# Kernel tuning notes

Hardware: AMD Instinct MI355X
Metric: run time of the kernel (lower is better)

## Reference

```python
import jax, jax.numpy as jnp
import numpy as np

TIME_STEP = 15
INIT_STATE = 0.01  # torch.full((B,H), 0.01)


def setup_inputs() -> dict:
    key = jax.random.key(0)
    k1, k2, k3, k4, k5 = jax.random.split(key, 5)
    B, IN, H = 2048, 2048, 1024
    scale_ih = 1.0 / np.sqrt(H)
    return {
        "x": jax.random.normal(k1, (B, IN), dtype=jnp.float32),
        "W_ih": jax.random.normal(k2, (4 * H, IN), dtype=jnp.float32) * scale_ih,
        "W_hh": jax.random.normal(k3, (4 * H, H), dtype=jnp.float32) * scale_ih,
        "b_ih": jax.random.normal(k4, (4 * H,), dtype=jnp.float32) * scale_ih,
        "b_hh": jax.random.normal(k5, (4 * H,), dtype=jnp.float32) * scale_ih,
    }


def reference(x, W_ih, W_hh, b_ih, b_hh):
    B = x.shape[0]
    H = W_hh.shape[1]
    # x is constant across steps -> precompute input-gate contribution once
    xg = x @ W_ih.T + b_ih  # [B, 4H]
    h0 = jnp.full((B, H), INIT_STATE, dtype=x.dtype)
    c0 = jnp.full((B, H), INIT_STATE, dtype=x.dtype)

    def step(carry, _):
        h, c = carry
        gates = xg + h @ W_hh.T + b_hh  # [B, 4H]
        i, f, g, o = jnp.split(gates, 4, axis=-1)
        i = jax.nn.sigmoid(i)
        f = jax.nn.sigmoid(f)
        g = jnp.tanh(g)
        o = jax.nn.sigmoid(o)
        c_new = f * c + i * g
        h_new = o * jnp.tanh(c_new)
        return (h_new, c_new), h_new

    _, hs = jax.lax.scan(step, (h0, c0), None, length=TIME_STEP)
    return hs  # [T, B, H]
```

## Files before the change

### kernel.cpp

```cpp
#include <hip/hip_runtime.h>
#include <hip/hip_bf16.h>

typedef float f32x4 __attribute__((ext_vector_type(4)));
typedef __bf16 bf16x8 __attribute__((ext_vector_type(8)));

#define B_SZ 2048
#define IN_SZ 2048
#define H_SZ 1024
#define G_SZ (4 * H_SZ)
#define T_STEPS 15
#define INIT_ST 0.01f

__device__ __forceinline__ float sigmoid_f(float x) { return 1.0f / (1.0f + __expf(-x)); }
__device__ __forceinline__ float tanh_f(float x)    { return 1.0f - 2.0f / (__expf(2.0f * x) + 1.0f); }

__device__ __forceinline__ void split8(f32x4 v0, f32x4 v1, bf16x8* h, bf16x8* l) {
  bf16x8 hv, lv;
  #pragma unroll
  for (int j = 0; j < 4; ++j) {
    float f = v0[j];
    __bf16 hb = (__bf16)f;
    hv[j] = hb;
    lv[j] = (__bf16)(f - (float)hb);
  }
  #pragma unroll
  for (int j = 0; j < 4; ++j) {
    float f = v1[j];
    __bf16 hb = (__bf16)f;
    hv[4 + j] = hb;
    lv[4 + j] = (__bf16)(f - (float)hb);
  }
  *h = hv;
  *l = lv;
}

__device__ __forceinline__ bf16x8 cvt8(f32x4 v0, f32x4 v1) {
  bf16x8 hv;
  #pragma unroll
  for (int j = 0; j < 4; ++j) hv[j] = (__bf16)v0[j];
  #pragma unroll
  for (int j = 0; j < 4; ++j) hv[4 + j] = (__bf16)v1[j];
  return hv;
}

__device__ __forceinline__ void gl16(const bf16x8* src, bf16x8* lds_base_uniform) {
  __builtin_amdgcn_global_load_lds(
      (const __attribute__((address_space(1))) void*)src,
      (__attribute__((address_space(3))) void*)lds_base_uniform, 16, 0, 0);
}

__global__ __launch_bounds__(256)
void repack_whh(const float* __restrict__ Whh, bf16x8* __restrict__ Wh)
{
  int cid = blockIdx.x * 256 + threadIdx.x;
  int s    = cid & 1023;
  int rest = cid >> 10;
  int ks   = rest & 31;
  int nt   = rest >> 5;
  int row  = s >> 2;
  int kc   = (s & 3) ^ (row & 3);
  int gate = row >> 6, col = row & 63;
  const float* src = Whh + (size_t)(gate * H_SZ + nt * 64 + col) * H_SZ + ks * 32 + kc * 8;
  Wh[cid] = cvt8(*(const f32x4*)src, *(const f32x4*)(src + 4));
}

__global__ __launch_bounds__(256)
void init_h0(bf16x8* __restrict__ hh, bf16x8* __restrict__ hl)
{
  int cid = blockIdx.x * 256 + threadIdx.x;
  __bf16 hi = (__bf16)INIT_ST;
  __bf16 lo = (__bf16)(INIT_ST - (float)hi);
  bf16x8 h, l;
  #pragma unroll
  for (int j = 0; j < 8; ++j) { h[j] = hi; l[j] = lo; }
  hh[cid] = h;
  hl[cid] = l;
}

__global__ __launch_bounds__(256, 2)
void xg_gemm(const float* __restrict__ x, const float* __restrict__ Wih,
             const float* __restrict__ bih, const float* __restrict__ bhh,
             float* __restrict__ xg)
{
  __shared__ bf16x8 Ah[128 * 4], Al[128 * 4], Bh[128 * 4], Bl[128 * 4];
  const int tid  = threadIdx.x;
  const int lane = tid & 63;
  const int wv   = tid >> 6;
  const int wm   = wv >> 1, wn = wv & 1;
  const int bm   = blockIdx.y * 128;
  const int bn   = blockIdx.x * 128;

  f32x4 acc[4][4] = {};

  for (int k0 = 0; k0 < IN_SZ; k0 += 32) {
    #pragma unroll
    for (int c = 0; c < 2; ++c) {
      int cid = tid + c * 256;
      int row = cid >> 2, kc = cid & 3;
      int idx = row * 4 + (kc ^ (row & 3));
      const float* srcA = x + (size_t)(bm + row) * IN_SZ + k0 + kc * 8;
      split8(*(const f32x4*)srcA, *(const f32x4*)(srcA + 4), &Ah[idx], &Al[idx]);
      const float* srcB = Wih + (size_t)(bn + row) * IN_SZ + k0 + kc * 8;
      split8(*(const f32x4*)srcB, *(const f32x4*)(srcB + 4), &Bh[idx], &Bl[idx]);
    }
    __syncthreads();

    const int kc = lane >> 4;
    bf16x8 ah[4], al[4], bh[4], bl[4];
    #pragma unroll
    for (int i = 0; i < 4; ++i) {
      int ra = wm * 64 + i * 16 + (lane & 15);
      int ia = ra * 4 + (kc ^ (ra & 3));
      ah[i] = Ah[ia]; al[i] = Al[ia];
      int rb = wn * 64 + i * 16 + (lane & 15);
      int ib = rb * 4 + (kc ^ (rb & 3));
      bh[i] = Bh[ib]; bl[i] = Bl[ib];
    }
    #pragma unroll
    for (int i = 0; i < 4; ++i)
      #pragma unroll
      for (int j = 0; j < 4; ++j) {
        acc[i][j] = __builtin_amdgcn_mfma_f32_16x16x32_bf16(ah[i], bh[j], acc[i][j], 0, 0, 0);
        acc[i][j] = __builtin_amdgcn_mfma_f32_16x16x32_bf16(ah[i], bl[j], acc[i][j], 0, 0, 0);
        acc[i][j] = __builtin_amdgcn_mfma_f32_16x16x32_bf16(al[i], bh[j], acc[i][j], 0, 0, 0);
      }
    __syncthreads();
  }

  #pragma unroll
  for (int i = 0; i < 4; ++i) {
    int m0 = bm + wm * 64 + i * 16 + ((lane >> 4) * 4);
    #pragma unroll
    for (int j = 0; j < 4; ++j) {
      int n = bn + wn * 64 + j * 16 + (lane & 15);
      float bb = bih[n] + bhh[n];
      #pragma unroll
      for (int r = 0; r < 4; ++r)
        xg[(size_t)(m0 + r) * G_SZ + n] = acc[i][j][r] + bb;
    }
  }
}

__global__ __launch_bounds__(256, 2)
void lstm_step(const bf16x8* __restrict__ hsh,
               const bf16x8* __restrict__ hsl,
               const bf16x8* __restrict__ Wh,
               const float* __restrict__ xg,
               float* __restrict__ cst,
               float* __restrict__ hout,
               bf16x8* __restrict__ hnh,
               bf16x8* __restrict__ hnl,
               int first)
{
  __shared__ __attribute__((aligned(16))) char smem[73728];
  bf16x8* L = (bf16x8*)smem;

  const int tid  = threadIdx.x;
  const int lane = tid & 63;
  const int wv   = tid >> 6;
  const int wg   = wv;

  const int bid  = blockIdx.x;
  const int wgid = (bid & 7) * 64 + (bid >> 3);
  const int nt   = wgid >> 5;
  const int mt   = wgid & 31;

  f32x4 acc[4][4] = {};
  const size_t abase = (size_t)mt * 32;
  const size_t bbase = (size_t)nt * 32;
  const int kc = lane >> 4;

  bf16x8 ahA[4], alA[4], bhA[4];
  bf16x8 ahB[4], alB[4], bhB[4];

#define STAGE(BUF, KS)                                                      \
  do {                                                                      \
    gl16(hsh + (abase + (KS)) * 256 + tid, L + (BUF) * 1536 + wv * 64);     \
    gl16(hsl + (abase + (KS)) * 256 + tid, L + (BUF) * 1536 + 256 + wv * 64); \
    const bf16x8* sb = Wh + (bbase + (KS)) * 1024;                          \
    gl16(sb + tid,       L + (BUF) * 1536 + 512 + wv * 64);                 \
    gl16(sb + 256 + tid, L + (BUF) * 1536 + 768 + wv * 64);                 \
    gl16(sb + 512 + tid, L + (BUF) * 1536 + 1024 + wv * 64);                \
    gl16(sb + 768 + tid, L + (BUF) * 1536 + 1280 + wv * 64);                \
  } while (0)

#define READF(S, BUF)                                                       \
  do {                                                                      \
    _Pragma("unroll")                                                       \
    for (int i = 0; i < 4; ++i) {                                           \
      int ra = i * 16 + (lane & 15);                                        \
      int ca = (BUF) * 1536 + ra * 4 + (kc ^ (ra & 3));                     \
      ah##S[i] = L[ca];                                                     \
      al##S[i] = L[ca + 256];                                               \
      int rb = wg * 64 + i * 16 + (lane & 15);                              \
      int cb = (BUF) * 1536 + 512 + rb * 4 + (kc ^ (rb & 3));               \
      bh##S[i] = L[cb];                                                     \
    }                                                                       \
  } while (0)

#define MFMAF(S)                                                            \
  do {                                                                      \
    __builtin_amdgcn_s_setprio(1);                                          \
    _Pragma("unroll")                                                       \
    for (int i = 0; i < 4; ++i)                                             \
      _Pragma("unroll")                                                     \
      for (int j = 0; j < 4; ++j) {                                         \
        acc[i][j] = __builtin_amdgcn_mfma_f32_16x16x32_bf16(ah##S[i], bh##S[j], acc[i][j], 0, 0, 0); \
        acc[i][j] = __builtin_amdgcn_mfma_f32_16x16x32_bf16(al##S[i], bh##S[j], acc[i][j], 0, 0, 0); \
      }                                                                     \
    __builtin_amdgcn_s_setprio(0);                                          \
  } while (0)

#define ITER(KS, SB, RB, RS, MS)                                            \
  do {                                                                      \
    asm volatile("s_waitcnt lgkmcnt(0)" ::: "memory");                      \
    asm volatile("s_waitcnt vmcnt(6)" ::: "memory");                        \
    __builtin_amdgcn_s_barrier();                                           \
    STAGE(SB, (KS) + 3);                                                    \
    READF(RS, RB);                                                          \
    MFMAF(MS);                                                              \
  } while (0)

  STAGE(0, 0);
  STAGE(1, 1);
  STAGE(2, 2);
  asm volatile("s_waitcnt vmcnt(12)" ::: "memory");
  __builtin_amdgcn_s_barrier();
  READF(A, 0);

  #pragma unroll 1
  for (int r6 = 0; r6 < 24; r6 += 6) {
    ITER(r6 + 0, 0, 1, B, A);
    ITER(r6 + 1, 1, 2, A, B);
    ITER(r6 + 2, 2, 0, B, A);
    ITER(r6 + 3, 0, 1, A, B);
    ITER(r6 + 4, 1, 2, B, A);
    ITER(r6 + 5, 2, 0, A, B);
  }
  ITER(24, 0, 1, B, A);
  ITER(25, 1, 2, A, B);
  ITER(26, 2, 0, B, A);
  ITER(27, 0, 1, A, B);
  ITER(28, 1, 2, B, A);
  asm volatile("s_waitcnt lgkmcnt(0)" ::: "memory");
  asm volatile("s_waitcnt vmcnt(6)" ::: "memory");
  __builtin_amdgcn_s_barrier();
  READF(A, 0);
  MFMAF(B);
  asm volatile("s_waitcnt lgkmcnt(0)" ::: "memory");
  asm volatile("s_waitcnt vmcnt(0)" ::: "memory");
  __builtin_amdgcn_s_barrier();
  READF(B, 1);
  MFMAF(A);
  MFMAF(B);
  __builtin_amdgcn_s_barrier();

#undef ITER
#undef MFMAF
#undef READF
#undef STAGE

  const int bm = mt * 64, bn = nt * 64;
  const int nl = (tid & 15) * 4;
  const int ml = (tid >> 4) * 4;

  f32x4 xgv[4][4], cv[4];
  #pragma unroll
  for (int r = 0; r < 4; ++r) {
    int m = bm + ml + r;
    const float* xr = xg + (size_t)m * G_SZ + bn + nl;
    #pragma unroll
    for (int g = 0; g < 4; ++g) xgv[g][r] = *(const f32x4*)(xr + g * H_SZ);
    if (first) cv[r] = (f32x4){INIT_ST, INIT_ST, INIT_ST, INIT_ST};
    else       cv[r] = *(const f32x4*)(cst + (size_t)m * H_SZ + bn + nl);
  }

  float* pre = (float*)smem;

  if (wg < 2) {
    #pragma unroll
    for (int i = 0; i < 4; ++i)
      #pragma unroll
      for (int j = 0; j < 4; ++j) {
        int n = j * 16 + (lane & 15);
        #pragma unroll
        for (int r = 0; r < 4; ++r) {
          int m = i * 16 + ((lane >> 4) * 4) + r;
          pre[(wg * 64 + m) * 68 + n] = acc[i][j][r];
        }
      }
  }
  asm volatile("s_waitcnt lgkmcnt(0)" ::: "memory");
  __builtin_amdgcn_s_barrier();

  f32x4 iv[4], fv[4];
  #pragma unroll
  for (int r = 0; r < 4; ++r) {
    int m = ml + r;
    f32x4 pi = *(const f32x4*)&pre[(0 * 64 + m) * 68 + nl];
    f32x4 pf = *(const f32x4*)&pre[(1 * 64 + m) * 68 + nl];
    #pragma unroll
    for (int j = 0; j < 4; ++j) {
      iv[r][j] = sigmoid_f(pi[j] + xgv[0][r][j]);
      fv[r][j] = sigmoid_f(pf[j] + xgv[1][r][j]);
    }
  }
  __builtin_amdgcn_s_barrier();

  if (wg >= 2) {
    #pragma unroll
    for (int i = 0; i < 4; ++i)
      #pragma unroll
      for (int j = 0; j < 4; ++j) {
        int n = j * 16 + (lane & 15);
        #pragma unroll
        for (int r = 0; r < 4; ++r) {
          int m = i * 16 + ((lane >> 4) * 4) + r;
          pre[((wg - 2) * 64 + m) * 68 + n] = acc[i][j][r];
        }
      }
  }
  asm volatile("s_waitcnt lgkmcnt(0)" ::: "memory");
  __builtin_amdgcn_s_barrier();

  __bf16* ph = (__bf16*)hnh;
  __bf16* pl = (__bf16*)hnl;
  #pragma unroll
  for (int r = 0; r < 4; ++r) {
    int m = ml + r;
    f32x4 pg = *(const f32x4*)&pre[(0 * 64 + m) * 68 + nl];
    f32x4 po = *(const f32x4*)&pre[(1 * 64 + m) * 68 + nl];
    f32x4 cnew, hv;
    #pragma unroll
    for (int j = 0; j < 4; ++j) {
      float gv = tanh_f(pg[j] + xgv[2][r][j]);
      float ov = sigmoid_f(po[j] + xgv[3][r][j]);
      cnew[j] = fv[r][j] * cv[r][j] + iv[r][j] * gv;
      hv[j]   = ov * tanh_f(cnew[j]);
    }
    int mg = bm + m;
    *(f32x4*)(cst  + (size_t)mg * H_SZ + bn + nl) = cnew;
    *(f32x4*)(hout + (size_t)mg * H_SZ + bn + nl) = hv;

    int nglob = bn + nl;
    int ks2 = nglob >> 5;
    int kc2 = (nglob >> 3) & 3;
    int eb  = nglob & 7;
    int s2  = m * 4 + (kc2 ^ (m & 3));
    size_t ci = (((size_t)mt * 32 + ks2) * 256 + s2) * 8 + eb;
    union { __bf16 b[4]; uint2 u; } uh, ul;
    #pragma unroll
    for (int j = 0; j < 4; ++j) {
      __bf16 hb = (__bf16)hv[j];
      uh.b[j] = hb;
      ul.b[j] = (__bf16)(hv[j] - (float)hb);
    }
    *(uint2*)(ph + ci) = uh.u;
    *(uint2*)(pl + ci) = ul.u;
  }
}

extern "C" void kernel_launch(void* const* d_in, const int* in_sizes, int n_in,
                              void* d_out, int out_size, void* d_ws, size_t ws_size,
                              hipStream_t stream)
{
  const float* x   = (const float*)d_in[0];
  const float* Wih = (const float*)d_in[1];
  const float* Whh = (const float*)d_in[2];
  const float* bih = (const float*)d_in[3];
  const float* bhh = (const float*)d_in[4];
  float* out = (float*)d_out;

  float*  xg  = (float*)d_ws;
  float*  cst = xg + (size_t)B_SZ * G_SZ;
  bf16x8* Wh  = (bf16x8*)(cst + (size_t)B_SZ * H_SZ);
  bf16x8* hAh = Wh + 524288;
  bf16x8* hAl = hAh + 262144;
  bf16x8* hBh = hAl + 262144;
  bf16x8* hBl = hBh + 262144;

  repack_whh<<<2048, 256, 0, stream>>>(Whh, Wh);
  init_h0<<<1024, 256, 0, stream>>>(hAh, hAl);
  xg_gemm<<<dim3(G_SZ / 128, B_SZ / 128), 256, 0, stream>>>(x, Wih, bih, bhh, xg);

  for (int t = 0; t < T_STEPS; ++t) {
    const bf16x8* rh = (t & 1) ? hBh : hAh;
    const bf16x8* rl = (t & 1) ? hBl : hAl;
    bf16x8* wh = (t & 1) ? hAh : hBh;
    bf16x8* wl = (t & 1) ? hAl : hBl;
    lstm_step<<<512, 256, 0, stream>>>(rh, rl, Wh, xg, cst,
                                       out + (size_t)t * B_SZ * H_SZ, wh, wl,
                                       t == 0 ? 1 : 0);
  }
}
```

Before: 869.4 us.

## Enlarge LSTM step tile to 128x256 and change LDS swizzle

```diff
diff --git a/kernel.cpp b/kernel.cpp
--- a/kernel.cpp
+++ b/kernel.cpp
@@ -48,6 +48,7 @@
       (const __attribute__((address_space(1))) void*)src,
       (__attribute__((address_space(3))) void*)lds_base_uniform, 16, 0, 0);
 }
+
 
 __global__ __launch_bounds__(256)
 void repack_whh(const float* __restrict__ Whh, bf16x8* __restrict__ Wh)
@@ -58,7 +59,7 @@
   int ks   = rest & 31;
   int nt   = rest >> 5;
   int row  = s >> 2;
-  int kc   = (s & 3) ^ (row & 3);
+  int kc   = (s & 3) ^ ((row >> 1) & 3);
   int gate = row >> 6, col = row & 63;
   const float* src = Whh + (size_t)(gate * H_SZ + nt * 64 + col) * H_SZ + ks * 32 + kc * 8;
   Wh[cid] = cvt8(*(const f32x4*)src, *(const f32x4*)(src + 4));
@@ -77,7 +78,7 @@
   hl[cid] = l;
 }
 
-__global__ __launch_bounds__(256, 2)
+__global__ __launch_bounds__(256, 4)
 void xg_gemm(const float* __restrict__ x, const float* __restrict__ Wih,
              const float* __restrict__ bih, const float* __restrict__ bhh,
              float* __restrict__ xg)
@@ -97,7 +98,7 @@
     for (int c = 0; c < 2; ++c) {
       int cid = tid + c * 256;
       int row = cid >> 2, kc = cid & 3;
-      int idx = row * 4 + (kc ^ (row & 3));
+      int idx = row * 4 + (kc ^ ((row >> 1) & 3));
       const float* srcA = x + (size_t)(bm + row) * IN_SZ + k0 + kc * 8;
       split8(*(const f32x4*)srcA, *(const f32x4*)(srcA + 4), &Ah[idx], &Al[idx]);
       const float* srcB = Wih + (size_t)(bn + row) * IN_SZ + k0 + kc * 8;
@@ -110,10 +111,10 @@
     #pragma unroll
     for (int i = 0; i < 4; ++i) {
       int ra = wm * 64 + i * 16 + (lane & 15);
-      int ia = ra * 4 + (kc ^ (ra & 3));
+      int ia = ra * 4 + (kc ^ ((ra >> 1) & 3));
       ah[i] = Ah[ia]; al[i] = Al[ia];
       int rb = wn * 64 + i * 16 + (lane & 15);
-      int ib = rb * 4 + (kc ^ (rb & 3));
+      int ib = rb * 4 + (kc ^ ((rb >> 1) & 3));
       bh[i] = Bh[ib]; bl[i] = Bl[ib];
     }
     #pragma unroll
@@ -141,7 +142,7 @@
   }
 }
 
-__global__ __launch_bounds__(256, 2)
+__global__ __launch_bounds__(256, 1)
 void lstm_step(const bf16x8* __restrict__ hsh,
                const bf16x8* __restrict__ hsl,
                const bf16x8* __restrict__ Wh,
@@ -152,79 +153,83 @@
                bf16x8* __restrict__ hnl,
                int first)
 {
-  __shared__ __attribute__((aligned(16))) char smem[73728];
+  __shared__ __attribute__((aligned(16))) char smem[98304];
   bf16x8* L = (bf16x8*)smem;
 
   const int tid  = threadIdx.x;
   const int lane = tid & 63;
   const int wv   = tid >> 6;
-  const int wg   = wv;
+  const int wm   = wv >> 1;
+  const int wn   = wv & 1;
 
   const int bid  = blockIdx.x;
-  const int wgid = (bid & 7) * 64 + (bid >> 3);
-  const int nt   = wgid >> 5;
-  const int mt   = wgid & 31;
-
-  f32x4 acc[4][4] = {};
-  const size_t abase = (size_t)mt * 32;
-  const size_t bbase = (size_t)nt * 32;
+  const int wgid = (bid & 7) * 32 + (bid >> 3);
+  const int nt   = wgid >> 4;
+  const int mt   = wgid & 15;
+
+  f32x4 acc[4][8] = {};
   const int kc = lane >> 4;
 
-  bf16x8 ahA[4], alA[4], bhA[4];
-  bf16x8 ahB[4], alB[4], bhB[4];
-
-#define STAGE(BUF, KS)                                                      \
-  do {                                                                      \
-    gl16(hsh + (abase + (KS)) * 256 + tid, L + (BUF) * 1536 + wv * 64);     \
-    gl16(hsl + (abase + (KS)) * 256 + tid, L + (BUF) * 1536 + 256 + wv * 64); \
-    const bf16x8* sb = Wh + (bbase + (KS)) * 1024;                          \
-    gl16(sb + tid,       L + (BUF) * 1536 + 512 + wv * 64);                 \
-    gl16(sb + 256 + tid, L + (BUF) * 1536 + 768 + wv * 64);                 \
-    gl16(sb + 512 + tid, L + (BUF) * 1536 + 1024 + wv * 64);                \
-    gl16(sb + 768 + tid, L + (BUF) * 1536 + 1280 + wv * 64);                \
+  bf16x8 ahA[4], alA[4], bhA[8];
+  bf16x8 ahB[4], alB[4], bhB[8];
+
+#define STAGE(BUF, KS)                                                        \
+  do {                                                                        \
+    gl16(hsh + ((size_t)(2 * mt)     * 32 + (KS)) * 256 + tid, L + (BUF) * 2048 +        wv * 64); \
+    gl16(hsh + ((size_t)(2 * mt + 1) * 32 + (KS)) * 256 + tid, L + (BUF) * 2048 + 256  + wv * 64); \
+    gl16(hsl + ((size_t)(2 * mt)     * 32 + (KS)) * 256 + tid, L + (BUF) * 2048 + 512  + wv * 64); \
+    gl16(hsl + ((size_t)(2 * mt + 1) * 32 + (KS)) * 256 + tid, L + (BUF) * 2048 + 768  + wv * 64); \
+    const bf16x8* sb = Wh + ((size_t)nt * 32 + (KS)) * 1024;                  \
+    gl16(sb + tid,       L + (BUF) * 2048 + 1024 + wv * 64);                  \
+    gl16(sb + 256 + tid, L + (BUF) * 2048 + 1280 + wv * 64);                  \
+    gl16(sb + 512 + tid, L + (BUF) * 2048 + 1536 + wv * 64);                  \
+    gl16(sb + 768 + tid, L + (BUF) * 2048 + 1792 + wv * 64);                  \
   } while (0)
 
-#define READF(S, BUF)                                                       \
-  do {                                                                      \
-    _Pragma("unroll")                                                       \
-    for (int i = 0; i < 4; ++i) {                                           \
-      int ra = i * 16 + (lane & 15);                                        \
-      int ca = (BUF) * 1536 + ra * 4 + (kc ^ (ra & 3));                     \
-      ah##S[i] = L[ca];                                                     \
-      al##S[i] = L[ca + 256];                                               \
-      int rb = wg * 64 + i * 16 + (lane & 15);                              \
-      int cb = (BUF) * 1536 + 512 + rb * 4 + (kc ^ (rb & 3));               \
-      bh##S[i] = L[cb];                                                     \
-    }                                                                       \
+#define READF(S, BUF)                                                         \
+  do {                                                                        \
+    _Pragma("unroll")                                                         \
+    for (int i = 0; i < 4; ++i) {                                             \
+      int ra = wm * 64 + i * 16 + (lane & 15);                                \
+      int ca = (BUF) * 2048 + ra * 4 + (kc ^ ((ra >> 1) & 3));                \
+      ah##S[i] = L[ca];                                                       \
+      al##S[i] = L[ca + 512];                                                 \
+    }                                                                         \
+    _Pragma("unroll")                                                         \
+    for (int j = 0; j < 8; ++j) {                                             \
+      int rb = wn * 128 + j * 16 + (lane & 15);                               \
+      int cb = (BUF) * 2048 + 1024 + rb * 4 + (kc ^ ((rb >> 1) & 3));         \
+      bh##S[j] = L[cb];                                                       \
+    }                                                                         \
   } while (0)
 
-#define MFMAF(S)                                                            \
-  do {                                                                      \
-    __builtin_amdgcn_s_setprio(1);                                          \
-    _Pragma("unroll")                                                       \
-    for (int i = 0; i < 4; ++i)                                             \
-      _Pragma("unroll")                                                     \
-      for (int j = 0; j < 4; ++j) {                                         \
+#define MFMAF(S)                                                              \
+  do {                                                                        \
+    __builtin_amdgcn_s_setprio(1);                                            \
+    _Pragma("unroll")                                                         \
+    for (int i = 0; i < 4; ++i)                                               \
+      _Pragma("unroll")                                                       \
+      for (int j = 0; j < 8; ++j) {                                           \
         acc[i][j] = __builtin_amdgcn_mfma_f32_16x16x32_bf16(ah##S[i], bh##S[j], acc[i][j], 0, 0, 0); \
         acc[i][j] = __builtin_amdgcn_mfma_f32_16x16x32_bf16(al##S[i], bh##S[j], acc[i][j], 0, 0, 0); \
-      }                                                                     \
-    __builtin_amdgcn_s_setprio(0);                                          \
+      }                                                                       \
+    __builtin_amdgcn_s_setprio(0);                                            \
   } while (0)
 
-#define ITER(KS, SB, RB, RS, MS)                                            \
-  do {                                                                      \
-    asm volatile("s_waitcnt lgkmcnt(0)" ::: "memory");                      \
-    asm volatile("s_waitcnt vmcnt(6)" ::: "memory");                        \
-    __builtin_amdgcn_s_barrier();                                           \
-    STAGE(SB, (KS) + 3);                                                    \
-    READF(RS, RB);                                                          \
-    MFMAF(MS);                                                              \
+#define ITER(KS, SB, RB, RS, MS)                                              \
+  do {                                                                        \
+    asm volatile("s_waitcnt lgkmcnt(0)" ::: "memory");                        \
+    asm volatile("s_waitcnt vmcnt(8)" ::: "memory");                          \
+    __builtin_amdgcn_s_barrier();                                             \
+    STAGE(SB, (KS) + 3);                                                      \
+    READF(RS, RB);                                                            \
+    MFMAF(MS);                                                                \
   } while (0)
 
   STAGE(0, 0);
   STAGE(1, 1);
   STAGE(2, 2);
-  asm volatile("s_waitcnt vmcnt(12)" ::: "memory");
+  asm volatile("s_waitcnt vmcnt(16)" ::: "memory");
   __builtin_amdgcn_s_barrier();
   READF(A, 0);
 
@@ -243,7 +248,7 @@
   ITER(27, 0, 1, A, B);
   ITER(28, 1, 2, B, A);
   asm volatile("s_waitcnt lgkmcnt(0)" ::: "memory");
-  asm volatile("s_waitcnt vmcnt(6)" ::: "memory");
+  asm volatile("s_waitcnt vmcnt(8)" ::: "memory");
   __builtin_amdgcn_s_barrier();
   READF(A, 0);
   MFMAF(B);
@@ -260,63 +265,57 @@
 #undef READF
 #undef STAGE
 
-  const int bm = mt * 64, bn = nt * 64;
+  const int bm = mt * 128, bn = nt * 64;
   const int nl = (tid & 15) * 4;
-  const int ml = (tid >> 4) * 4;
-
-  f32x4 xgv[4][4], cv[4];
-  #pragma unroll
-  for (int r = 0; r < 4; ++r) {
-    int m = bm + ml + r;
-    const float* xr = xg + (size_t)m * G_SZ + bn + nl;
-    #pragma unroll
-    for (int g = 0; g < 4; ++g) xgv[g][r] = *(const f32x4*)(xr + g * H_SZ);
-    if (first) cv[r] = (f32x4){INIT_ST, INIT_ST, INIT_ST, INIT_ST};
-    else       cv[r] = *(const f32x4*)(cst + (size_t)m * H_SZ + bn + nl);
-  }
+  const int ml = (tid >> 4) * 8;
 
   float* pre = (float*)smem;
 
-  if (wg < 2) {
+  if (wn == 0) {
     #pragma unroll
     for (int i = 0; i < 4; ++i)
       #pragma unroll
-      for (int j = 0; j < 4; ++j) {
-        int n = j * 16 + (lane & 15);
+      for (int j = 0; j < 8; ++j) {
+        int slot = j >> 2;
+        int c = (j & 3) * 16 + (lane & 15);
         #pragma unroll
         for (int r = 0; r < 4; ++r) {
-          int m = i * 16 + ((lane >> 4) * 4) + r;
-          pre[(wg * 64 + m) * 68 + n] = acc[i][j][r];
+          int m = wm * 64 + i * 16 + ((lane >> 4) * 4) + r;
+          pre[(slot * 128 + m) * 68 + c] = acc[i][j][r];
         }
       }
   }
   asm volatile("s_waitcnt lgkmcnt(0)" ::: "memory");
   __builtin_amdgcn_s_barrier();
 
-  f32x4 iv[4], fv[4];
-  #pragma unroll
-  for (int r = 0; r < 4; ++r) {
-    int m = ml + r;
-    f32x4 pi = *(const f32x4*)&pre[(0 * 64 + m) * 68 + nl];
-    f32x4 pf = *(const f32x4*)&pre[(1 * 64 + m) * 68 + nl];
+  f32x4 iv[8], fv[8];
+  #pragma unroll
+  for (int r8 = 0; r8 < 8; ++r8) {
+    int m = ml + r8;
+    f32x4 pi = *(const f32x4*)&pre[(0 * 128 + m) * 68 + nl];
+    f32x4 pf = *(const f32x4*)&pre[(1 * 128 + m) * 68 + nl];
+    const float* xr = xg + (size_t)(bm + m) * G_SZ + bn + nl;
+    f32x4 x0 = *(const f32x4*)xr;
+    f32x4 x1 = *(const f32x4*)(xr + H_SZ);
     #pragma unroll
     for (int j = 0; j < 4; ++j) {
-      iv[r][j] = sigmoid_f(pi[j] + xgv[0][r][j]);
-      fv[r][j] = sigmoid_f(pf[j] + xgv[1][r][j]);
-    }
-  }
-  __builtin_amdgcn_s_barrier();
-
-  if (wg >= 2) {
+      iv[r8][j] = sigmoid_f(pi[j] + x0[j]);
+      fv[r8][j] = sigmoid_f(pf[j] + x1[j]);
+    }
+  }
+  __builtin_amdgcn_s_barrier();
+
+  if (wn == 1) {
     #pragma unroll
     for (int i = 0; i < 4; ++i)
       #pragma unroll
-      for (int j = 0; j < 4; ++j) {
-        int n = j * 16 + (lane & 15);
+      for (int j = 0; j < 8; ++j) {
+        int slot = j >> 2;
+        int c = (j & 3) * 16 + (lane & 15);
         #pragma unroll
         for (int r = 0; r < 4; ++r) {
-          int m = i * 16 + ((lane >> 4) * 4) + r;
-          pre[((wg - 2) * 64 + m) * 68 + n] = acc[i][j][r];
+          int m = wm * 64 + i * 16 + ((lane >> 4) * 4) + r;
+          pre[(slot * 128 + m) * 68 + c] = acc[i][j][r];
         }
       }
   }
@@ -326,19 +325,25 @@
   __bf16* ph = (__bf16*)hnh;
   __bf16* pl = (__bf16*)hnl;
   #pragma unroll
-  for (int r = 0; r < 4; ++r) {
-    int m = ml + r;
-    f32x4 pg = *(const f32x4*)&pre[(0 * 64 + m) * 68 + nl];
-    f32x4 po = *(const f32x4*)&pre[(1 * 64 + m) * 68 + nl];
+  for (int r8 = 0; r8 < 8; ++r8) {
+    int m = ml + r8;
+    int mg = bm + m;
+    f32x4 pg = *(const f32x4*)&pre[(0 * 128 + m) * 68 + nl];
+    f32x4 po = *(const f32x4*)&pre[(1 * 128 + m) * 68 + nl];
+    const float* xr = xg + (size_t)mg * G_SZ + bn + nl;
+    f32x4 x2 = *(const f32x4*)(xr + 2 * H_SZ);
+    f32x4 x3 = *(const f32x4*)(xr + 3 * H_SZ);
+    f32x4 cvv;
+    if (first) cvv = (f32x4){INIT_ST, INIT_ST, INIT_ST, INIT_ST};
+    else       cvv = *(const f32x4*)(cst + (size_t)mg * H_SZ + bn + nl);
     f32x4 cnew, hv;
     #pragma unroll
     for (int j = 0; j < 4; ++j) {
-      float gv = tanh_f(pg[j] + xgv[2][r][j]);
-      float ov = sigmoid_f(po[j] + xgv[3][r][j]);
-      cnew[j] = fv[r][j] * cv[r][j] + iv[r][j] * gv;
+      float gv = tanh_f(pg[j] + x2[j]);
+      float ov = sigmoid_f(po[j] + x3[j]);
+      cnew[j] = fv[r8][j] * cvv[j] + iv[r8][j] * gv;
       hv[j]   = ov * tanh_f(cnew[j]);
     }
-    int mg = bm + m;
     *(f32x4*)(cst  + (size_t)mg * H_SZ + bn + nl) = cnew;
     *(f32x4*)(hout + (size_t)mg * H_SZ + bn + nl) = hv;
 
@@ -346,8 +351,10 @@
     int ks2 = nglob >> 5;
     int kc2 = (nglob >> 3) & 3;
     int eb  = nglob & 7;
-    int s2  = m * 4 + (kc2 ^ (m & 3));
-    size_t ci = (((size_t)mt * 32 + ks2) * 256 + s2) * 8 + eb;
+    int r64 = m & 63;
+    int mt64 = 2 * mt + (m >> 6);
+    int s2  = r64 * 4 + (kc2 ^ ((r64 >> 1) & 3));
+    size_t ci = (((size_t)mt64 * 32 + ks2) * 256 + s2) * 8 + eb;
     union { __bf16 b[4]; uint2 u; } uh, ul;
     #pragma unroll
     for (int j = 0; j < 4; ++j) {
@@ -388,7 +395,7 @@
     const bf16x8* rl = (t & 1) ? hBl : hAl;
     bf16x8* wh = (t & 1) ? hAh : hBh;
     bf16x8* wl = (t & 1) ? hAl : hBl;
-    lstm_step<<<512, 256, 0, stream>>>(rh, rl, Wh, xg, cst,
+    lstm_step<<<256, 256, 0, stream>>>(rh, rl, Wh, xg, cst,
                                        out + (size_t)t * B_SZ * H_SZ, wh, wl,
                                        t == 0 ? 1 : 0);
   }
```

Measured after the change: 933.9 us. 7.4% more time.
